# Kernel optimization log

Hardware: AMD Instinct MI355X
Metric: run time of the kernel (lower is better)

The kernel has to match this reference:

```python
import jax, jax.numpy as jnp
import numpy as np
import math

N_EMBD = 64
HEAD_SIZE = 64
B, T = 16, 2048


def setup_inputs() -> dict:
    key = jax.random.key(0)
    k1, k2, k3, k4 = jax.random.split(key, 4)
    inputs = jax.random.normal(k1, (B, T, N_EMBD), dtype=jnp.float32)
    # Causal mask: True where attention is NOT allowed (upper triangle),
    # matching masked_fill_(mask, -1e9) with mask = ~tril.
    mask = jnp.triu(jnp.ones((T, T), dtype=bool), k=1)
    # nn.Linear(n_embd, head_size, bias=False) weights, stored as
    # (n_embd, head_size) so projection is inputs @ W (== x @ W_torch.T).
    scale = 1.0 / math.sqrt(N_EMBD)
    Wq = jax.random.uniform(k2, (N_EMBD, HEAD_SIZE), jnp.float32, -scale, scale)
    Wk = jax.random.uniform(k3, (N_EMBD, HEAD_SIZE), jnp.float32, -scale, scale)
    Wv = jax.random.uniform(k4, (N_EMBD, HEAD_SIZE), jnp.float32, -scale, scale)
    return {"inputs": inputs, "mask": mask, "Wq": Wq, "Wk": Wk, "Wv": Wv}


def reference(inputs, mask, Wq, Wk, Wv):
    # inputs: (B, T, n_embd); mask: (T, T) bool broadcast over batch
    q = inputs @ Wq  # (B, T, H)
    k = inputs @ Wk  # (B, T, H)
    v = inputs @ Wv  # (B, T, H)
    inv_sqrt_h = 1.0 / math.sqrt(HEAD_SIZE)
    scores = jnp.einsum('bth,bsh->bts', q, k) * inv_sqrt_h  # (B, T, T)
    scores = jnp.where(mask, jnp.float32(-1e9), scores)
    attention = jax.nn.softmax(scores, axis=-1)
    out = jnp.einsum('bts,bsh->bth', attention, v)  # (B, T, H)
    return out
```

## Files before the change

kernel.cpp:

```cpp
#include <hip/hip_runtime.h>
#include <stdint.h>


typedef __bf16 bf16x8 __attribute__((ext_vector_type(8)));
typedef __bf16 bf16x4 __attribute__((ext_vector_type(4)));
typedef float f32x4 __attribute__((ext_vector_type(4)));

#define QSCALE 0.18033688011112042f
#define MFMA16(a, b, c) __builtin_amdgcn_mfma_f32_16x16x32_bf16((a), (b), (c), 0, 0, 0)

__device__ __forceinline__ unsigned short f2bf(float f) {
  union { float f; unsigned u; } x; x.f = f;
  unsigned r = x.u + 0x7fffu + ((x.u >> 16) & 1u);
  return (unsigned short)(r >> 16);
}

__device__ __forceinline__ int swz(int row, int bytecol) {
  return row * 128 + (bytecol ^ ((row & 7) << 4));
}
__device__ __forceinline__ int swzV(int row, int bytecol) {
  return row * 256 + (bytecol ^ ((row & 7) << 4));
}
__device__ __forceinline__ bf16x8 frag(const unsigned short* base, int row, int kf, int lane) {
  int off = swz(row, kf * 64 + ((lane >> 4) << 4));
  return *(const bf16x8*)((const char*)base + off);
}

__global__ __launch_bounds__(256, 2) void proj_kernel(
    const float* __restrict__ X, const float* __restrict__ Wq,
    const float* __restrict__ Wk, const float* __restrict__ Wv,
    unsigned short* __restrict__ Qg, unsigned short* __restrict__ Kg,
    unsigned short* __restrict__ Vtg) {
  __shared__ __align__(16) unsigned short Xs[64 * 64];
  __shared__ __align__(16) unsigned short Ws[3 * 64 * 64];
  const int tid = threadIdx.x, lane = tid & 63, w = tid >> 6;
  const int ln = lane & 15, g = lane >> 4;
  const long grow0 = (long)blockIdx.x * 64;
  const int b = (int)(grow0 >> 11);
  const int tin0 = (int)(grow0 & 2047);

  {
    const int r = tid >> 2, c = tid & 3;
    const float* src = X + (grow0 + r) * 64 + c * 16;
    float4 f0 = *(const float4*)src;
    float4 f1 = *(const float4*)(src + 4);
    float4 f2 = *(const float4*)(src + 8);
    float4 f3 = *(const float4*)(src + 12);
    uint4 d0, d1;
    d0.x = f2bf(f0.x) | ((unsigned)f2bf(f0.y) << 16);
    d0.y = f2bf(f0.z) | ((unsigned)f2bf(f0.w) << 16);
    d0.z = f2bf(f1.x) | ((unsigned)f2bf(f1.y) << 16);
    d0.w = f2bf(f1.z) | ((unsigned)f2bf(f1.w) << 16);
    d1.x = f2bf(f2.x) | ((unsigned)f2bf(f2.y) << 16);
    d1.y = f2bf(f2.z) | ((unsigned)f2bf(f2.w) << 16);
    d1.z = f2bf(f3.x) | ((unsigned)f2bf(f3.y) << 16);
    d1.w = f2bf(f3.z) | ((unsigned)f2bf(f3.w) << 16);
    *(uint4*)((char*)Xs + swz(r, c * 32)) = d0;
    *(uint4*)((char*)Xs + swz(r, c * 32 + 16)) = d1;
  }
  for (int c = tid; c < 3 * 4096; c += 256) {
    const int mat = c >> 12, rr = c & 4095;
    const int e = rr >> 6, hh = rr & 63;
    const float* wsrc = (mat == 0) ? Wq : (mat == 1) ? Wk : Wv;
    *(unsigned short*)((char*)(Ws + mat * 4096) + swz(hh, e * 2)) = f2bf(wsrc[rr]);
  }
  __syncthreads();

  const f32x4 zero = {0.f, 0.f, 0.f, 0.f};
#pragma unroll
  for (int i = 0; i < 3; ++i) {
    const int task = w * 3 + i;
    const int mat = task >> 2, s = task & 3;
    const unsigned short* wbase = Ws + mat * 4096;
    if (mat < 2) {
      bf16x8 a0 = frag(Xs, s * 16 + ln, 0, lane);
      bf16x8 a1 = frag(Xs, s * 16 + ln, 1, lane);
      unsigned short* dst = mat ? Kg : Qg;
#pragma unroll
      for (int nt = 0; nt < 4; ++nt) {
        bf16x8 b0 = frag(wbase, nt * 16 + ln, 0, lane);
        bf16x8 b1 = frag(wbase, nt * 16 + ln, 1, lane);
        f32x4 acc = MFMA16(a0, b0, zero);
        acc = MFMA16(a1, b1, acc);
        long row0 = grow0 + s * 16 + g * 4;
        int col = nt * 16 + ln;
#pragma unroll
        for (int k = 0; k < 4; ++k) {
          float v = acc[k];
          if (mat == 0) v *= QSCALE;
          dst[(row0 + k) * 64 + col] = f2bf(v);
        }
      }
    } else {
      bf16x8 a0 = frag(wbase, s * 16 + ln, 0, lane);
      bf16x8 a1 = frag(wbase, s * 16 + ln, 1, lane);
#pragma unroll
      for (int nt = 0; nt < 4; ++nt) {
        bf16x8 b0 = frag(Xs, nt * 16 + ln, 0, lane);
        bf16x8 b1 = frag(Xs, nt * 16 + ln, 1, lane);
        f32x4 acc = MFMA16(a0, b0, zero);
        acc = MFMA16(a1, b1, acc);
        int t = tin0 + nt * 16 + ln;
        int h0 = s * 16 + g * 4;
#pragma unroll
        for (int k = 0; k < 4; ++k)
          Vtg[((long)(b * 64 + h0 + k)) * 2048 + t] = f2bf(acc[k]);
      }
    }
  }
}

__global__ __launch_bounds__(512, 4) void attn7_kernel(
    const unsigned short* __restrict__ Qg, const unsigned short* __restrict__ Kg,
    const unsigned short* __restrict__ Vtg, float* __restrict__ Og) {
  __shared__ __align__(16) unsigned char smem[65536];

  const int bid = blockIdx.x;
  const int xcd = bid & 7, idx = bid >> 3;
  const int b = (xcd << 1) + (idx & 1);
  const int m = idx >> 1;
  const int qt = (idx & 1) ? (31 - m) : m;
  const int q0 = qt * 64;
  const int ns = (qt >> 1) + 1;

  const int tid = threadIdx.x;
  const int lane = tid & 63, w = tid >> 6;
  const int g = lane >> 4, ln = lane & 15;
  const int kvq = w & 3, qh = w >> 2;

  const unsigned short* qrow = Qg + ((long)b * 2048 + q0 + qh * 32) * 64;
  const bf16x8 qb00 = *(const bf16x8*)(qrow + ln * 64 + g * 8);
  const bf16x8 qb01 = *(const bf16x8*)(qrow + ln * 64 + 32 + g * 8);
  const bf16x8 qb10 = *(const bf16x8*)(qrow + (16 + ln) * 64 + g * 8);
  const bf16x8 qb11 = *(const bf16x8*)(qrow + (16 + ln) * 64 + 32 + g * 8);

  const unsigned short* kbase = Kg + (long)b * 2048 * 64;
  const unsigned short* vbase = Vtg + (long)b * 64 * 2048;

  const int rk = tid >> 2, ck = tid & 3;
  const int rv = tid >> 3, cv = tid & 7;

  const f32x4 zero = {0.f, 0.f, 0.f, 0.f};
  f32x4 o0[4], o1[4];
#pragma unroll
  for (int nt = 0; nt < 4; ++nt) { o0[nt] = zero; o1[nt] = zero; }
  float den0 = 0.f, den1 = 0.f;

  {
    const unsigned short* kg = kbase + (long)rk * 64 + ck * 16;
    uint4 k0 = *(const uint4*)kg;
    uint4 k1 = *(const uint4*)(kg + 8);
    const unsigned short* vg = vbase + (long)rv * 2048 + cv * 16;
    uint4 v0 = *(const uint4*)vg;
    uint4 v1 = *(const uint4*)(vg + 8);
    unsigned char* Kb = smem;
    unsigned char* Vb = smem + 16384;
    *(uint4*)(Kb + swz(rk, ck * 32)) = k0;
    *(uint4*)(Kb + swz(rk, ck * 32 + 16)) = k1;
    *(uint4*)(Vb + swzV(rv, cv * 32)) = v0;
    *(uint4*)(Vb + swzV(rv, cv * 32 + 16)) = v1;
  }
  __syncthreads();

  int cur = 0;
  for (int t = 0; t < ns; ++t) {
    const int kv0 = t * 128;
    const bool pre = (t + 1 < ns);
    uint4 k0, k1, v0, v1;
    if (pre) {
      const int kv0n = kv0 + 128;
      const unsigned short* kg = kbase + (long)(kv0n + rk) * 64 + ck * 16;
      k0 = *(const uint4*)kg;
      k1 = *(const uint4*)(kg + 8);
      const unsigned short* vg = vbase + (long)rv * 2048 + kv0n + cv * 16;
      v0 = *(const uint4*)vg;
      v1 = *(const uint4*)(vg + 8);
    }

    const unsigned short* Kb = (const unsigned short*)(smem + cur * 32768);
    const unsigned char*  Vb = smem + cur * 32768 + 16384;

    bf16x8 ka00 = frag(Kb, kvq * 32 + ln,      0, lane);
    bf16x8 ka01 = frag(Kb, kvq * 32 + ln,      1, lane);
    bf16x8 ka10 = frag(Kb, kvq * 32 + 16 + ln, 0, lane);
    bf16x8 ka11 = frag(Kb, kvq * 32 + 16 + ln, 1, lane);

    bf16x8 vb[4];
#pragma unroll
    for (int nt = 0; nt < 4; ++nt) {
      int row = nt * 16 + ln;
      bf16x4 lo = *(const bf16x4*)(Vb + swzV(row, kvq * 64 + g * 8));
      bf16x4 hi = *(const bf16x4*)(Vb + swzV(row, kvq * 64 + 32 + g * 8));
      vb[nt] = __builtin_shufflevector(lo, hi, 0, 1, 2, 3, 4, 5, 6, 7);
    }

    __builtin_amdgcn_s_setprio(1);
    f32x4 st00 = MFMA16(ka00, qb00, zero);  st00 = MFMA16(ka01, qb01, st00);
    f32x4 st01 = MFMA16(ka00, qb10, zero);  st01 = MFMA16(ka01, qb11, st01);
    f32x4 st10 = MFMA16(ka10, qb00, zero);  st10 = MFMA16(ka11, qb01, st10);
    f32x4 st11 = MFMA16(ka10, qb10, zero);  st11 = MFMA16(ka11, qb11, st11);
    __builtin_amdgcn_s_setprio(0);

    if (t == ns - 1) {
      const int qg0 = q0 + qh * 32 + ln;
      const int qg1 = qg0 + 16;
      const int kvb = kv0 + kvq * 32 + g * 4;
#pragma unroll
      for (int i = 0; i < 4; ++i) {
        if (kvb + i > qg0)      st00[i] = -1e30f;
        if (kvb + i > qg1)      st01[i] = -1e30f;
        if (kvb + 16 + i > qg0) st10[i] = -1e30f;
        if (kvb + 16 + i > qg1) st11[i] = -1e30f;
      }
    }

    bf16x8 pa0, pa1;
#pragma unroll
    for (int i = 0; i < 4; ++i) {
      float p00 = exp2f(st00[i]);
      float p10 = exp2f(st10[i]);
      float p01 = exp2f(st01[i]);
      float p11 = exp2f(st11[i]);
      den0 += p00 + p10;
      den1 += p01 + p11;
      pa0[i] = (__bf16)p00;  pa0[4 + i] = (__bf16)p10;
      pa1[i] = (__bf16)p01;  pa1[4 + i] = (__bf16)p11;
    }

    __builtin_amdgcn_s_setprio(1);
#pragma unroll
    for (int nt = 0; nt < 4; ++nt) {
      o0[nt] = MFMA16(pa0, vb[nt], o0[nt]);
      o1[nt] = MFMA16(pa1, vb[nt], o1[nt]);
    }
    __builtin_amdgcn_s_setprio(0);

    if (pre) {
      unsigned char* Kn = smem + (cur ^ 1) * 32768;
      unsigned char* Vn = Kn + 16384;
      *(uint4*)(Kn + swz(rk, ck * 32)) = k0;
      *(uint4*)(Kn + swz(rk, ck * 32 + 16)) = k1;
      *(uint4*)(Vn + swzV(rv, cv * 32)) = v0;
      *(uint4*)(Vn + swzV(rv, cv * 32 + 16)) = v1;
    }
    __syncthreads();
    cur ^= 1;
  }

  den0 += __shfl_xor(den0, 16);
  den0 += __shfl_xor(den0, 32);
  den1 += __shfl_xor(den1, 16);
  den1 += __shfl_xor(den1, 32);

  float* Olds = (float*)smem;
  float* Dlds = (float*)(smem + 34816);
  if (lane < 16) {
    Dlds[kvq * 64 + qh * 32 + ln] = den0;
    Dlds[kvq * 64 + qh * 32 + 16 + ln] = den1;
  }
#pragma unroll
  for (int phase = 0; phase < 2; ++phase) {
    if (phase) __syncthreads();
    if (qh == phase) {
#pragma unroll
      for (int nt = 0; nt < 4; ++nt)
#pragma unroll
        for (int i = 0; i < 4; ++i) {
          Olds[(kvq * 32 + g * 4 + i) * 68 + nt * 16 + ln] = o0[nt][i];
          Olds[(kvq * 32 + 16 + g * 4 + i) * 68 + nt * 16 + ln] = o1[nt][i];
        }
    }
    __syncthreads();
    const int q = tid >> 4;
    const int d0 = (tid & 15) * 4;
    const int qq = phase * 32 + q;
    float dd = Dlds[qq] + Dlds[64 + qq] + Dlds[128 + qq] + Dlds[192 + qq];
    float inv = 1.0f / dd;
    float4 r0 = *(float4*)&Olds[(0 * 32 + q) * 68 + d0];
    float4 r1 = *(float4*)&Olds[(1 * 32 + q) * 68 + d0];
    float4 r2 = *(float4*)&Olds[(2 * 32 + q) * 68 + d0];
    float4 r3 = *(float4*)&Olds[(3 * 32 + q) * 68 + d0];
    float4 out;
    out.x = (r0.x + r1.x + r2.x + r3.x) * inv;
    out.y = (r0.y + r1.y + r2.y + r3.y) * inv;
    out.z = (r0.z + r1.z + r2.z + r3.z) * inv;
    out.w = (r0.w + r1.w + r2.w + r3.w) * inv;
    *(float4*)(Og + ((long)b * 2048 + q0 + qq) * 64 + d0) = out;
  }
}

extern "C" void kernel_launch(void* const* d_in, const int* in_sizes, int n_in,
                              void* d_out, int out_size, void* d_ws, size_t ws_size,
                              hipStream_t stream) {
  const float* X  = (const float*)d_in[0];
  const float* Wq = (const float*)d_in[2];
  const float* Wk = (const float*)d_in[3];
  const float* Wv = (const float*)d_in[4];

  unsigned short* Qg  = (unsigned short*)d_ws;
  unsigned short* Kg  = Qg + 2097152;
  unsigned short* Vtg = Kg + 2097152;

  proj_kernel<<<512, 256, 0, stream>>>(X, Wq, Wk, Wv, Qg, Kg, Vtg);
  attn7_kernel<<<512, 512, 0, stream>>>(Qg, Kg, Vtg, (float*)d_out);
}
```

Measured before the change: 46.85 us.

## Restructure attention into smaller tiles with direct global-to-LDS async loads

Rewrites the attention kernel to use 32-query tiles with 256-thread blocks (1024 blocks) and 64-key steps, reducing LDS to about 35KB per block so more blocks fit per CU. K/V tiles are now fetched with global_load_lds directly into swizzled shared memory instead of staging through registers, which frees registers and removes the ds_write pass. The cross-warp output reduction shrinks to two partials. This trades more loop iterations and barriers per block for finer load balance and higher occupancy.

```diff
diff --git a/kernel.cpp b/kernel.cpp
--- a/kernel.cpp
+++ b/kernel.cpp
@@ -18,12 +18,15 @@
 __device__ __forceinline__ int swz(int row, int bytecol) {
   return row * 128 + (bytecol ^ ((row & 7) << 4));
 }
-__device__ __forceinline__ int swzV(int row, int bytecol) {
-  return row * 256 + (bytecol ^ ((row & 7) << 4));
-}
 __device__ __forceinline__ bf16x8 frag(const unsigned short* base, int row, int kf, int lane) {
   int off = swz(row, kf * 64 + ((lane >> 4) << 4));
   return *(const bf16x8*)((const char*)base + off);
+}
+
+__device__ __forceinline__ void gload_lds16(const unsigned short* g, unsigned short* l) {
+  __builtin_amdgcn_global_load_lds(
+      (const __attribute__((address_space(1))) unsigned int*)g,
+      (__attribute__((address_space(3))) unsigned int*)l, 16, 0, 0);
 }
 
 __global__ __launch_bounds__(256, 2) void proj_kernel(
@@ -110,183 +113,153 @@
   }
 }
 
-__global__ __launch_bounds__(512, 4) void attn7_kernel(
+__global__ __launch_bounds__(256, 4) void attn8_kernel(
     const unsigned short* __restrict__ Qg, const unsigned short* __restrict__ Kg,
     const unsigned short* __restrict__ Vtg, float* __restrict__ Og) {
-  __shared__ __align__(16) unsigned char smem[65536];
+  __shared__ __align__(16) unsigned char smem[35840];
 
   const int bid = blockIdx.x;
-  const int xcd = bid & 7, idx = bid >> 3;
-  const int b = (xcd << 1) + (idx & 1);
-  const int m = idx >> 1;
-  const int qt = (idx & 1) ? (31 - m) : m;
-  const int q0 = qt * 64;
-  const int ns = (qt >> 1) + 1;
+  const int slot = bid >> 3;
+  const int b = ((bid & 7) << 1) + (slot & 1);
+  const int j = slot >> 1;
+  const int qt = (j & 1) ? (j >> 1) : 63 - (j >> 1);
+  const int q0 = qt * 32;
+  const int ns = (q0 + 95) >> 6;
 
   const int tid = threadIdx.x;
   const int lane = tid & 63, w = tid >> 6;
   const int g = lane >> 4, ln = lane & 15;
-  const int kvq = w & 3, qh = w >> 2;
-
-  const unsigned short* qrow = Qg + ((long)b * 2048 + q0 + qh * 32) * 64;
-  const bf16x8 qb00 = *(const bf16x8*)(qrow + ln * 64 + g * 8);
-  const bf16x8 qb01 = *(const bf16x8*)(qrow + ln * 64 + 32 + g * 8);
-  const bf16x8 qb10 = *(const bf16x8*)(qrow + (16 + ln) * 64 + g * 8);
-  const bf16x8 qb11 = *(const bf16x8*)(qrow + (16 + ln) * 64 + 32 + g * 8);
+  const int h = w & 1, qh = w >> 1;
+
+  const unsigned short* qrow = Qg + ((long)b * 2048 + q0 + qh * 16 + ln) * 64;
+  const bf16x8 qb0 = *(const bf16x8*)(qrow + g * 8);
+  const bf16x8 qb1 = *(const bf16x8*)(qrow + 32 + g * 8);
 
   const unsigned short* kbase = Kg + (long)b * 2048 * 64;
   const unsigned short* vbase = Vtg + (long)b * 64 * 2048;
 
-  const int rk = tid >> 2, ck = tid & 3;
-  const int rv = tid >> 3, cv = tid & 7;
+  const int sw32 = (w & 1) * 32;
+  const int cxor = ((lane & 7) ^ ((lane >> 3) & 7)) * 8;
+  const int klane = (lane >> 3) * 64 + cxor;
+  const int vlane = (lane >> 3) * 2048 + cxor;
 
   const f32x4 zero = {0.f, 0.f, 0.f, 0.f};
-  f32x4 o0[4], o1[4];
-#pragma unroll
-  for (int nt = 0; nt < 4; ++nt) { o0[nt] = zero; o1[nt] = zero; }
-  float den0 = 0.f, den1 = 0.f;
-
-  {
-    const unsigned short* kg = kbase + (long)rk * 64 + ck * 16;
-    uint4 k0 = *(const uint4*)kg;
-    uint4 k1 = *(const uint4*)(kg + 8);
-    const unsigned short* vg = vbase + (long)rv * 2048 + cv * 16;
-    uint4 v0 = *(const uint4*)vg;
-    uint4 v1 = *(const uint4*)(vg + 8);
-    unsigned char* Kb = smem;
-    unsigned char* Vb = smem + 16384;
-    *(uint4*)(Kb + swz(rk, ck * 32)) = k0;
-    *(uint4*)(Kb + swz(rk, ck * 32 + 16)) = k1;
-    *(uint4*)(Vb + swzV(rv, cv * 32)) = v0;
-    *(uint4*)(Vb + swzV(rv, cv * 32 + 16)) = v1;
+  f32x4 o[4];
+#pragma unroll
+  for (int nt = 0; nt < 4; ++nt) o[nt] = zero;
+  float den = 0.f;
+
+  if (w < 2) {
+#pragma unroll
+    for (int i = 0; i < 4; ++i)
+      gload_lds16(kbase + (long)(sw32 + i * 8) * 64 + klane,
+                  (unsigned short*)smem + (sw32 + i * 8) * 64);
+  } else {
+#pragma unroll
+    for (int i = 0; i < 4; ++i)
+      gload_lds16(vbase + (long)(sw32 + i * 8) * 2048 + vlane,
+                  (unsigned short*)(smem + 8192) + (sw32 + i * 8) * 64);
   }
   __syncthreads();
 
   int cur = 0;
   for (int t = 0; t < ns; ++t) {
-    const int kv0 = t * 128;
-    const bool pre = (t + 1 < ns);
-    uint4 k0, k1, v0, v1;
-    if (pre) {
-      const int kv0n = kv0 + 128;
-      const unsigned short* kg = kbase + (long)(kv0n + rk) * 64 + ck * 16;
-      k0 = *(const uint4*)kg;
-      k1 = *(const uint4*)(kg + 8);
-      const unsigned short* vg = vbase + (long)rv * 2048 + kv0n + cv * 16;
-      v0 = *(const uint4*)vg;
-      v1 = *(const uint4*)(vg + 8);
-    }
-
-    const unsigned short* Kb = (const unsigned short*)(smem + cur * 32768);
-    const unsigned char*  Vb = smem + cur * 32768 + 16384;
-
-    bf16x8 ka00 = frag(Kb, kvq * 32 + ln,      0, lane);
-    bf16x8 ka01 = frag(Kb, kvq * 32 + ln,      1, lane);
-    bf16x8 ka10 = frag(Kb, kvq * 32 + 16 + ln, 0, lane);
-    bf16x8 ka11 = frag(Kb, kvq * 32 + 16 + ln, 1, lane);
+    const int kv0 = t * 64;
+    if (t + 1 < ns) {
+      const int kvn = kv0 + 64;
+      unsigned short* dstK = (unsigned short*)(smem + (cur ^ 1) * 16384);
+      unsigned short* dstV = (unsigned short*)(smem + (cur ^ 1) * 16384 + 8192);
+      if (w < 2) {
+#pragma unroll
+        for (int i = 0; i < 4; ++i)
+          gload_lds16(kbase + (long)(kvn + sw32 + i * 8) * 64 + klane,
+                      dstK + (sw32 + i * 8) * 64);
+      } else {
+#pragma unroll
+        for (int i = 0; i < 4; ++i)
+          gload_lds16(vbase + (long)(sw32 + i * 8) * 2048 + kvn + vlane,
+                      dstV + (sw32 + i * 8) * 64);
+      }
+    }
+
+    const unsigned short* Kb = (const unsigned short*)(smem + cur * 16384);
+    const unsigned char*  Vb = smem + cur * 16384 + 8192;
+
+    bf16x8 ka00 = frag(Kb, h * 32 + ln,      0, lane);
+    bf16x8 ka01 = frag(Kb, h * 32 + ln,      1, lane);
+    bf16x8 ka10 = frag(Kb, h * 32 + 16 + ln, 0, lane);
+    bf16x8 ka11 = frag(Kb, h * 32 + 16 + ln, 1, lane);
 
     bf16x8 vb[4];
 #pragma unroll
     for (int nt = 0; nt < 4; ++nt) {
       int row = nt * 16 + ln;
-      bf16x4 lo = *(const bf16x4*)(Vb + swzV(row, kvq * 64 + g * 8));
-      bf16x4 hi = *(const bf16x4*)(Vb + swzV(row, kvq * 64 + 32 + g * 8));
+      bf16x4 lo = *(const bf16x4*)(Vb + swz(row, h * 64 + g * 8));
+      bf16x4 hi = *(const bf16x4*)(Vb + swz(row, h * 64 + 32 + g * 8));
       vb[nt] = __builtin_shufflevector(lo, hi, 0, 1, 2, 3, 4, 5, 6, 7);
     }
 
     __builtin_amdgcn_s_setprio(1);
-    f32x4 st00 = MFMA16(ka00, qb00, zero);  st00 = MFMA16(ka01, qb01, st00);
-    f32x4 st01 = MFMA16(ka00, qb10, zero);  st01 = MFMA16(ka01, qb11, st01);
-    f32x4 st10 = MFMA16(ka10, qb00, zero);  st10 = MFMA16(ka11, qb01, st10);
-    f32x4 st11 = MFMA16(ka10, qb10, zero);  st11 = MFMA16(ka11, qb11, st11);
+    f32x4 st0 = MFMA16(ka00, qb0, zero);  st0 = MFMA16(ka01, qb1, st0);
+    f32x4 st1 = MFMA16(ka10, qb0, zero);  st1 = MFMA16(ka11, qb1, st1);
     __builtin_amdgcn_s_setprio(0);
 
     if (t == ns - 1) {
-      const int qg0 = q0 + qh * 32 + ln;
-      const int qg1 = qg0 + 16;
-      const int kvb = kv0 + kvq * 32 + g * 4;
+      const int qg = q0 + qh * 16 + ln;
+      const int kvb = kv0 + h * 32 + g * 4;
 #pragma unroll
       for (int i = 0; i < 4; ++i) {
-        if (kvb + i > qg0)      st00[i] = -1e30f;
-        if (kvb + i > qg1)      st01[i] = -1e30f;
-        if (kvb + 16 + i > qg0) st10[i] = -1e30f;
-        if (kvb + 16 + i > qg1) st11[i] = -1e30f;
-      }
-    }
-
-    bf16x8 pa0, pa1;
+        if (kvb + i > qg)      st0[i] = -1e30f;
+        if (kvb + 16 + i > qg) st1[i] = -1e30f;
+      }
+    }
+
+    bf16x8 pa;
 #pragma unroll
     for (int i = 0; i < 4; ++i) {
-      float p00 = exp2f(st00[i]);
-      float p10 = exp2f(st10[i]);
-      float p01 = exp2f(st01[i]);
-      float p11 = exp2f(st11[i]);
-      den0 += p00 + p10;
-      den1 += p01 + p11;
-      pa0[i] = (__bf16)p00;  pa0[4 + i] = (__bf16)p10;
-      pa1[i] = (__bf16)p01;  pa1[4 + i] = (__bf16)p11;
+      float p0 = exp2f(st0[i]);
+      float p1 = exp2f(st1[i]);
+      den += p0 + p1;
+      pa[i] = (__bf16)p0;
+      pa[4 + i] = (__bf16)p1;
     }
 
     __builtin_amdgcn_s_setprio(1);
 #pragma unroll
-    for (int nt = 0; nt < 4; ++nt) {
-      o0[nt] = MFMA16(pa0, vb[nt], o0[nt]);
-      o1[nt] = MFMA16(pa1, vb[nt], o1[nt]);
-    }
+    for (int nt = 0; nt < 4; ++nt)
+      o[nt] = MFMA16(pa, vb[nt], o[nt]);
     __builtin_amdgcn_s_setprio(0);
 
-    if (pre) {
-      unsigned char* Kn = smem + (cur ^ 1) * 32768;
-      unsigned char* Vn = Kn + 16384;
-      *(uint4*)(Kn + swz(rk, ck * 32)) = k0;
-      *(uint4*)(Kn + swz(rk, ck * 32 + 16)) = k1;
-      *(uint4*)(Vn + swzV(rv, cv * 32)) = v0;
-      *(uint4*)(Vn + swzV(rv, cv * 32 + 16)) = v1;
-    }
     __syncthreads();
     cur ^= 1;
   }
 
-  den0 += __shfl_xor(den0, 16);
-  den0 += __shfl_xor(den0, 32);
-  den1 += __shfl_xor(den1, 16);
-  den1 += __shfl_xor(den1, 32);
+  den += __shfl_xor(den, 16);
+  den += __shfl_xor(den, 32);
 
   float* Olds = (float*)smem;
   float* Dlds = (float*)(smem + 34816);
-  if (lane < 16) {
-    Dlds[kvq * 64 + qh * 32 + ln] = den0;
-    Dlds[kvq * 64 + qh * 32 + 16 + ln] = den1;
-  }
-#pragma unroll
-  for (int phase = 0; phase < 2; ++phase) {
-    if (phase) __syncthreads();
-    if (qh == phase) {
-#pragma unroll
-      for (int nt = 0; nt < 4; ++nt)
-#pragma unroll
-        for (int i = 0; i < 4; ++i) {
-          Olds[(kvq * 32 + g * 4 + i) * 68 + nt * 16 + ln] = o0[nt][i];
-          Olds[(kvq * 32 + 16 + g * 4 + i) * 68 + nt * 16 + ln] = o1[nt][i];
-        }
-    }
-    __syncthreads();
-    const int q = tid >> 4;
-    const int d0 = (tid & 15) * 4;
-    const int qq = phase * 32 + q;
-    float dd = Dlds[qq] + Dlds[64 + qq] + Dlds[128 + qq] + Dlds[192 + qq];
-    float inv = 1.0f / dd;
-    float4 r0 = *(float4*)&Olds[(0 * 32 + q) * 68 + d0];
-    float4 r1 = *(float4*)&Olds[(1 * 32 + q) * 68 + d0];
-    float4 r2 = *(float4*)&Olds[(2 * 32 + q) * 68 + d0];
-    float4 r3 = *(float4*)&Olds[(3 * 32 + q) * 68 + d0];
-    float4 out;
-    out.x = (r0.x + r1.x + r2.x + r3.x) * inv;
-    out.y = (r0.y + r1.y + r2.y + r3.y) * inv;
-    out.z = (r0.z + r1.z + r2.z + r3.z) * inv;
-    out.w = (r0.w + r1.w + r2.w + r3.w) * inv;
-    *(float4*)(Og + ((long)b * 2048 + q0 + qq) * 64 + d0) = out;
-  }
+#pragma unroll
+  for (int nt = 0; nt < 4; ++nt)
+#pragma unroll
+    for (int i = 0; i < 4; ++i)
+      Olds[(w * 16 + g * 4 + i) * 68 + nt * 16 + ln] = o[nt][i];
+  if (lane < 16) Dlds[w * 16 + ln] = den;
+  __syncthreads();
+
+  const int q = tid >> 3;
+  const int qhx = q >> 4, r = q & 15;
+  const int d0 = (tid & 7) * 8;
+  float dd = Dlds[(qhx * 2) * 16 + r] + Dlds[(qhx * 2 + 1) * 16 + r];
+  float inv = 1.0f / dd;
+  float acc[8];
+#pragma unroll
+  for (int e = 0; e < 8; ++e)
+    acc[e] = (Olds[((qhx * 2) * 16 + r) * 68 + d0 + e] +
+              Olds[((qhx * 2 + 1) * 16 + r) * 68 + d0 + e]) * inv;
+  float* outp = Og + ((long)b * 2048 + q0 + q) * 64 + d0;
+  *(float4*)outp = make_float4(acc[0], acc[1], acc[2], acc[3]);
+  *(float4*)(outp + 4) = make_float4(acc[4], acc[5], acc[6], acc[7]);
 }
 
 extern "C" void kernel_launch(void* const* d_in, const int* in_sizes, int n_in,
@@ -302,5 +275,5 @@
   unsigned short* Vtg = Kg + 2097152;
 
   proj_kernel<<<512, 256, 0, stream>>>(X, Wq, Wk, Wv, Qg, Kg, Vtg);
-  attn7_kernel<<<512, 512, 0, stream>>>(Qg, Kg, Vtg, (float*)d_out);
-}
+  attn8_kernel<<<1024, 256, 0, stream>>>(Qg, Kg, Vtg, (float*)d_out);
+}
```

New measurement: 47.60 us. Within noise of the previous version (+1.6%).
